# Kernel tuning notes

Hardware: AMD Instinct MI355X
Metric: run time of the kernel (lower is better)

## Reference

```python
import jax, jax.numpy as jnp
import numpy as np
from jax import lax

N = 2; C_IN = 256
H0, W0 = 100, 152
H1, W1 = 50, 76
DYN_CH = 34            # 4 init_offset + 4 bound_pt_offset + 18 semantic_pt_offset + 8 reg_aggr_attn
REG_CH = 4             # 4 boundary points x 1 channel each
NUM_CLASSES = 80
SEM_PTS = 9
CLS_CH = SEM_PTS * NUM_CLASSES
BOUND_PTS = 4
RATIO = 0.5            # LIMIT_BOUND_POINT_OFFSET_RATIO

_BASE = np.array([[1,0,0,0],[0,1,0,0],[0.5,0,0.5,0],
                  [0,0.5,0,0.5],[0,0,1,0],[0,0,0,1]], np.float32)
BOUND_MAT = jnp.asarray(_BASE[[0,3,2,1,4,3,2,5]])                      # (8,4) box -> cross-shaped 4 pts
SEM_MAT = jnp.asarray(_BASE[[0,1,0,3,0,5,2,1,2,3,2,5,4,1,4,3,4,5]])    # (18,4) box -> 3x3 pts
BOUND_OFF_IDX = jnp.array([1, 2, 5, 6])   # tangential coordinate channel of each boundary point
LOC_IDX = jnp.array([0, 3, 4, 7])         # box-side coordinate channel of each boundary point

def conv3x3(x, w, b):
    y = lax.conv_general_dilated(x, w, (1, 1), 'SAME',
                                 dimension_numbers=('NCHW', 'OIHW', 'NCHW'))
    return y + b[None, :, None, None]

def conv1x1(x, w):
    return jnp.einsum('oi,nihw->nohw', w[:, :, 0, 0], x)

def pred_collect(fmap, pts, point_num, reduce_points, bias=None):
    # Bilinearly sample per-point channel groups of fmap at dynamic point locations.
    # fmap: (N, P*c, Hm, Wm); pts: (N, 2P, H, W) with (x, y) pairs per point.
    Nb, C, Hm, Wm = fmap.shape
    P = point_num; c = C // P
    H, W = pts.shape[2], pts.shape[3]
    fm = fmap.reshape(Nb, P, c, Hm, Wm)
    pg = pts.reshape(Nb, P, 2, H, W)
    def sample(f, pt):  # f: (c, Hm, Wm), pt: (2, H, W)
        x = jnp.clip(pt[0], 0.0, Wm - 1.0)
        y = jnp.clip(pt[1], 0.0, Hm - 1.0)
        x0 = jnp.floor(x); y0 = jnp.floor(y)
        fx = x - x0; fy = y - y0
        x0i = x0.astype(jnp.int32); y0i = y0.astype(jnp.int32)
        x1i = jnp.minimum(x0i + 1, Wm - 1); y1i = jnp.minimum(y0i + 1, Hm - 1)
        v00 = f[:, y0i, x0i]; v01 = f[:, y0i, x1i]
        v10 = f[:, y1i, x0i]; v11 = f[:, y1i, x1i]
        return v00*(1-fx)*(1-fy) + v01*fx*(1-fy) + v10*(1-fx)*fy + v11*fx*fy
    vals = jax.vmap(jax.vmap(sample))(fm, pg)  # (N, P, c, H, W)
    if reduce_points:
        out = vals.sum(axis=1)
        if bias is not None:
            out = out + bias[None, :, None, None]
        return out
    return vals.reshape(Nb, P * c, H, W)

def head_forward(reg_feats, cls_feats, anchors, dyn_w, dyn_b, reg_w, cls_w, cls_b):
    reg_maps = [conv1x1(x, reg_w) for x in reg_feats]
    cls_maps = [conv1x1(x, cls_w) for x in cls_feats]
    cls_scores, coarse_boxes, reg_boxes = [], [], []
    for i, (reg_feat, anchor) in enumerate(zip(reg_feats, anchors)):
        Nb, _, H, W = reg_feat.shape
        pred = conv3x3(reg_feat, dyn_w, dyn_b)
        init_off, bpt_off, spt_off, attn = jnp.split(pred, [4, 8, 26], axis=1)
        coarse = anchor + init_off                                  # (N,4,H,W) = (x1,y1,x2,y2)
        # straight-through clamp of boundary-point tangential offsets to +-wh/2*ratio
        bpt_off = bpt_off.reshape(Nb, 2, 2, 1, H, W)
        wh = jnp.stack([coarse[:, 3] - coarse[:, 1],
                        coarse[:, 2] - coarse[:, 0]], axis=1) / 2 * RATIO  # (N,2,H,W) [h,w]
        thres = wh[:, None, :, None]                                # (N,1,2,1,H,W)
        extra = jnp.maximum(bpt_off - thres, 0.0) + jnp.minimum(bpt_off + thres, 0.0)
        bpt_off = (bpt_off - lax.stop_gradient(extra)).reshape(Nb, 4, H, W)
        bound_pt = lax.stop_gradient(jnp.einsum('oc,nchw->nohw', BOUND_MAT, coarse))
        bound_pt = bound_pt.at[:, BOUND_OFF_IDX].add(bpt_off)       # (N,8,H,W)
        bound_pt_loc = bound_pt[:, LOC_IDX]                         # (N,4,H,W)
        reg_val = pred_collect(reg_maps[i], bound_pt, BOUND_PTS, False)  # (N,4,H,W)
        if i > 0:
            attn_sm = jax.nn.softmax(attn.reshape(Nb, BOUND_PTS, 2, H, W), axis=2)
            reg_hi = reg_val.reshape(Nb, BOUND_PTS, 1, 1, H, W)
            reg_lo = pred_collect(reg_maps[i - 1], bound_pt * 2, BOUND_PTS, False)
            reg_lo = reg_lo.reshape(Nb, BOUND_PTS, 1, 1, H, W) * 0.5
            reg_val = (jnp.concatenate([reg_lo, reg_hi], axis=2)
                       * attn_sm[:, :, :, None]).sum(axis=2).reshape(Nb, -1, H, W)
        reg_box = (lax.stop_gradient(bound_pt_loc) + reg_val).reshape(Nb, 4, -1, H, W).mean(axis=2)
        sem_pt = lax.stop_gradient(jnp.einsum('oc,nchw->nohw', SEM_MAT, coarse)) + spt_off
        cls_score = pred_collect(cls_maps[i], sem_pt, SEM_PTS, True, cls_b)  # (N,80,H,W)
        cls_scores.append(cls_score); coarse_boxes.append(coarse); reg_boxes.append(reg_box)
    return cls_scores, coarse_boxes, reg_boxes

def make_anchor(H, W):
    gy, gx = jnp.meshgrid(jnp.arange(H, dtype=jnp.float32),
                          jnp.arange(W, dtype=jnp.float32), indexing='ij')
    a = jnp.stack([gx - 4.0, gy - 4.0, gx + 4.0, gy + 4.0], axis=0)
    return jnp.broadcast_to(a[None], (N, 4, H, W))

def setup_inputs() -> dict:
    key = jax.random.key(0)
    ks = jax.random.split(key, 7)
    return {
        "reg_feat0": jax.random.normal(ks[0], (N, C_IN, H0, W0), jnp.float32),
        "reg_feat1": jax.random.normal(ks[1], (N, C_IN, H1, W1), jnp.float32),
        "cls_feat0": jax.random.normal(ks[2], (N, C_IN, H0, W0), jnp.float32),
        "cls_feat1": jax.random.normal(ks[3], (N, C_IN, H1, W1), jnp.float32),
        "anchor0": make_anchor(H0, W0),
        "anchor1": make_anchor(H1, W1),
        "dyn_w": jax.random.normal(ks[4], (DYN_CH, C_IN, 3, 3), jnp.float32) * 0.01,
        "dyn_b": jnp.zeros((DYN_CH,), jnp.float32),
        "reg_w": jax.random.normal(ks[5], (REG_CH, C_IN, 1, 1), jnp.float32) * 0.05,
        "cls_w": jax.random.normal(ks[6], (CLS_CH, C_IN, 1, 1), jnp.float32) * 0.05,
        "cls_b": jnp.zeros((NUM_CLASSES,), jnp.float32),
    }

def reference(reg_feat0, reg_feat1, cls_feat0, cls_feat1, anchor0, anchor1,
              dyn_w, dyn_b, reg_w, cls_w, cls_b):
    cls_scores, coarse_boxes, reg_boxes = head_forward(
        [reg_feat0, reg_feat1], [cls_feat0, cls_feat1], [anchor0, anchor1],
        dyn_w, dyn_b, reg_w, cls_w, cls_b)
    return (*cls_scores, *coarse_boxes, *reg_boxes)
```

## Files before the change

kernel.cpp:

```cpp
#include <hip/hip_runtime.h>
#include <hip/hip_bf16.h>
#include <cstdint>

#define N_BATCH 2
#define C_IN 256
#define DYN_CH 34
#define CLS_CH 720
#define NUM_CLASSES 80
#define NCOMB 48

#define P0c 15200
#define P1c 3800
#define M0c 30400
#define M1c 7600
#define MT0c 119
#define MT1c 30
#define CT0c 475
#define CT1c 119

typedef __attribute__((ext_vector_type(8))) short short8;
typedef __attribute__((ext_vector_type(4))) float f32x4;

typedef const unsigned int __attribute__((address_space(1)))* gas1_t;
typedef unsigned int __attribute__((address_space(3)))* las3_t;

__device__ __forceinline__ void async_ld16(const void* g, void* l) {
  __builtin_amdgcn_global_load_lds((gas1_t)g, (las3_t)l, 16, 0, 0);
}

__global__ __launch_bounds__(256) void pack_feat(
    const float* __restrict__ cls0, const float* __restrict__ cls1,
    const float* __restrict__ reg0, const float* __restrict__ reg1,
    const float* __restrict__ cls_w, const float* __restrict__ dyn_w,
    const float* __restrict__ reg_w, __hip_bfloat16* __restrict__ a0,
    __hip_bfloat16* __restrict__ a1, __hip_bfloat16* __restrict__ r0,
    __hip_bfloat16* __restrict__ r1, __hip_bfloat16* __restrict__ bpack,
    __hip_bfloat16* __restrict__ wpack) {
  int b = blockIdx.x;
  if (b >= 2384) {
    b -= 2384;
    if (b < 90) {
      int u = b * 256 + threadIdx.x;
      if (u >= 9 * 32 * 80) return;
      int ntile = u / 2560;
      int rem = u % 2560;
      int kcg = rem / 80;
      int ochl = rem % 80;
      int och = ntile * 80 + ochl;
      const float* wr = cls_w + (size_t)och * C_IN + kcg * 8;
      __hip_bfloat16 tmp[8];
#pragma unroll
      for (int c = 0; c < 8; ++c) tmp[c] = __float2bfloat16(wr[c]);
      *(uint4*)(bpack + (size_t)u * 8) = *(const uint4*)tmp;
    } else {
      int u = (b - 90) * 256 + threadIdx.x;
      if (u >= 13824) return;
      int j = u / 768;
      int r = u % 768;
      int n = r / 16;
      int s = r % 16;
      int ku = j * 16 + (s ^ (n & 7));
      int k0 = ku * 8;
      int tap = k0 >> 8;
      int c0 = k0 & 255;
      __hip_bfloat16 tmp[8];
#pragma unroll
      for (int i = 0; i < 8; ++i) {
        int c = c0 + i;
        float v = 0.f;
        if (n < DYN_CH) v = dyn_w[((size_t)n * C_IN + c) * 9 + tap];
        else if (n < DYN_CH + 4 && tap == 4)
          v = reg_w[(size_t)(n - DYN_CH) * C_IN + c];
        tmp[i] = __float2bfloat16(v);
      }
      *(uint4*)(wpack + (size_t)u * 8) = *(const uint4*)tmp;
    }
    return;
  }
  int j = b & 7;
  int mtg = b >> 3;
  const float* src;
  __hip_bfloat16* dst;
  int P, Mtot, mtile;
  if (mtg < 119)      { src = cls0; dst = a0; P = P0c; Mtot = M0c; mtile = mtg; }
  else if (mtg < 149) { src = cls1; dst = a1; P = P1c; Mtot = M1c; mtile = mtg - 119; }
  else if (mtg < 268) { src = reg0; dst = r0; P = P0c; Mtot = M0c; mtile = mtg - 149; }
  else                { src = reg1; dst = r1; P = P1c; Mtot = M1c; mtile = mtg - 268; }
  int wave = threadIdx.x >> 6;
  int lane = threadIdx.x & 63;
  int kcg = j * 4 + wave;
  int c0 = kcg * 8;
  int m4 = mtile * 256 + lane * 4;
  uint4* du = (uint4*)dst + (size_t)mtile * 8192 + (size_t)kcg * 256 + lane * 4;
  if (m4 < Mtot) {
    int n = m4 / P;
    int p = m4 - n * P;
    const float* sp = src + ((size_t)n * C_IN + c0) * P + p;
    float4 f[8];
#pragma unroll
    for (int c = 0; c < 8; ++c) f[c] = *(const float4*)(sp + (size_t)c * P);
#pragma unroll
    for (int i = 0; i < 4; ++i) {
      union { uint4 u; __hip_bfloat16 h[8]; } o;
#pragma unroll
      for (int c = 0; c < 8; ++c) {
        float v = (i == 0) ? f[c].x : (i == 1) ? f[c].y : (i == 2) ? f[c].z : f[c].w;
        o.h[c] = __float2bfloat16(v);
      }
      du[i] = o.u;
    }
  } else {
    uint4 z = {0u, 0u, 0u, 0u};
#pragma unroll
    for (int i = 0; i < 4; ++i) du[i] = z;
  }
}

__global__ __launch_bounds__(256) void cls_gemm_mfma(
    const uint4* __restrict__ Ap0, const uint4* __restrict__ Ap1,
    const uint4* __restrict__ Bp, __hip_bfloat16* __restrict__ out0,
    __hip_bfloat16* __restrict__ out1) {
  __shared__ uint4 Ash[1024];
  __shared__ uint4 Bsh[320];
  int bb = blockIdx.x;
  int g = bb & 7;
  int loc = bb >> 3;
  int lm = loc / 9;
  int ntile = loc - lm * 9;
  int mtile = g * 19 + lm;
  if (mtile >= MT0c + MT1c) return;
  int tid = threadIdx.x;
  int wave = tid >> 6;
  int lane = tid & 63;
  int l15 = lane & 15;
  int kq = lane >> 4;

  const uint4* Ap;
  __hip_bfloat16* out;
  int Mtot;
  if (mtile < MT0c) { Ap = Ap0; out = out0; Mtot = M0c; }
  else              { mtile -= MT0c; Ap = Ap1; out = out1; Mtot = M1c; }

  const uint4* Ab = Ap + (size_t)mtile * 8192;
  const uint4* Bb = Bp + (size_t)ntile * 2560;

  f32x4 acc[4][5];
#pragma unroll
  for (int i = 0; i < 4; ++i)
#pragma unroll
    for (int j = 0; j < 5; ++j) acc[i][j] = (f32x4)0.f;

  for (int kb = 0; kb < 8; ++kb) {
    const uint4* Aslab = Ab + kb * 1024;
#pragma unroll
    for (int i = 0; i < 4; ++i) {
      int j = wave * 4 + i;
      async_ld16(Aslab + j * 64 + lane, &Ash[j * 64]);
    }
    const uint4* Bslab = Bb + kb * 320;
    for (int j = wave; j < 5; j += 4) {
      async_ld16(Bslab + j * 64 + lane, &Bsh[j * 64]);
    }
    __syncthreads();

    short8 a[4], b[5];
    const uint4* Ar = &Ash[kq * 256 + wave * 64 + l15];
#pragma unroll
    for (int mi = 0; mi < 4; ++mi) a[mi] = *(const short8*)&Ar[mi * 16];
    const uint4* Br = &Bsh[kq * 80 + l15];
#pragma unroll
    for (int ni = 0; ni < 5; ++ni) b[ni] = *(const short8*)&Br[ni * 16];
#pragma unroll
    for (int mi = 0; mi < 4; ++mi)
#pragma unroll
      for (int ni = 0; ni < 5; ++ni)
        acc[mi][ni] = __builtin_amdgcn_mfma_f32_16x16x32_bf16(
            a[mi], b[ni], acc[mi][ni], 0, 0, 0);
    __syncthreads();
  }

  int gbase = mtile * 256 + wave * 64;
#pragma unroll
  for (int mi = 0; mi < 4; ++mi) {
#pragma unroll
    for (int r = 0; r < 4; ++r) {
      int gg = gbase + mi * 16 + kq * 4 + r;
      if (gg >= Mtot) continue;
      __hip_bfloat16* orow = out + (size_t)gg * CLS_CH + ntile * 80 + l15;
#pragma unroll
      for (int ni = 0; ni < 5; ++ni)
        orow[ni * 16] = __float2bfloat16(acc[mi][ni][r]);
    }
  }
}

__global__ __launch_bounds__(256) void dyn_reg_conv_mfma(
    const uint4* __restrict__ rp0, const uint4* __restrict__ rp1,
    const uint4* __restrict__ wp, float* __restrict__ part0,
    float* __restrict__ part1) {
  __shared__ uint4 Bs[768];
  int tid = threadIdx.x;
  int wave = tid >> 6;
  int lane = tid & 63;
  int l15 = lane & 15;
  int kq = lane >> 4;
  int seg = blockIdx.y;
  int bx = blockIdx.x;

  const uint4* rp;
  float* part;
  int Mtot, P, W, H;
  if (bx < CT0c) { rp = rp0; part = part0; Mtot = M0c; P = P0c; W = 152; H = 100; }
  else { bx -= CT0c; rp = rp1; part = part1; Mtot = M1c; P = P1c; W = 76; H = 50; }

  int m = bx * 64 + wave * 16 + l15;
  bool mval = (m < Mtot);
  int mc = mval ? m : 0;
  int n = mc / P;
  int rem = mc - n * P;
  int y = rem / W;
  int x = rem - y * W;

  f32x4 acc[3];
#pragma unroll
  for (int i = 0; i < 3; ++i) acc[i] = (f32x4)0.f;

  for (int jj = 0; jj < 6; ++jj) {
    int j = seg * 6 + jj;
    const uint4* wsrc = wp + (size_t)j * 768 + wave * 192;
#pragma unroll
    for (int i = 0; i < 3; ++i)
      async_ld16(wsrc + i * 64 + lane, &Bs[wave * 192 + i * 64]);

    int tap = j >> 1;
    int cb8 = (j & 1) * 16;
    int dy = tap / 3 - 1, dx = tap % 3 - 1;
    int sy = y + dy, sx = x + dx;
    bool val = mval && ((unsigned)sy < (unsigned)H) && ((unsigned)sx < (unsigned)W);
    int sm = m + dy * W + dx;
    int smc = val ? sm : 0;
    size_t tbase = (size_t)(smc >> 8) * 8192 + (smc & 255);
    uint4 a[4];
#pragma unroll
    for (int t = 0; t < 4; ++t) {
      uint4 v = {0u, 0u, 0u, 0u};
      if (val) v = rp[tbase + (size_t)(cb8 + t * 4 + kq) * 256];
      a[t] = v;
    }
    __syncthreads();
#pragma unroll
    for (int t = 0; t < 4; ++t) {
#pragma unroll
      for (int ni = 0; ni < 3; ++ni) {
        int nn = ni * 16 + l15;
        short8 bf = *(const short8*)&Bs[nn * 16 + ((t * 4 + kq) ^ (nn & 7))];
        acc[ni] = __builtin_amdgcn_mfma_f32_16x16x32_bf16(
            *(short8*)&a[t], bf, acc[ni], 0, 0, 0);
      }
    }
    __syncthreads();
  }

  int mrow = bx * 64 + wave * 16 + kq * 4;
#pragma unroll
  for (int r = 0; r < 4; ++r) {
    int mm = mrow + r;
    if (mm >= Mtot) continue;
    float* dst = part + ((size_t)seg * Mtot + mm) * NCOMB + l15;
#pragma unroll
    for (int ni = 0; ni < 3; ++ni) dst[ni * 16] = acc[ni][r];
  }
}

__device__ __forceinline__ float samp48(const float* __restrict__ part,
                                        int Mtot, int nbase, int W, int H,
                                        float px, float py, int ch) {
  float xc = fminf(fmaxf(px, 0.f), (float)(W - 1));
  float yc = fminf(fmaxf(py, 0.f), (float)(H - 1));
  float x0f = floorf(xc), y0f = floorf(yc);
  float fx = xc - x0f, fy = yc - y0f;
  int x0 = (int)x0f, y0 = (int)y0f;
  int x1 = min(x0 + 1, W - 1), y1 = min(y0 + 1, H - 1);
  size_t m00 = (size_t)(nbase + y0 * W + x0);
  size_t m01 = (size_t)(nbase + y0 * W + x1);
  size_t m10 = (size_t)(nbase + y1 * W + x0);
  size_t m11 = (size_t)(nbase + y1 * W + x1);
  float v00 = 0.f, v01 = 0.f, v10 = 0.f, v11 = 0.f;
#pragma unroll
  for (int s = 0; s < 3; ++s) {
    size_t off = (size_t)s * Mtot;
    v00 += part[(off + m00) * NCOMB + ch];
    v01 += part[(off + m01) * NCOMB + ch];
    v10 += part[(off + m10) * NCOMB + ch];
    v11 += part[(off + m11) * NCOMB + ch];
  }
  return v00 * (1.f - fx) * (1.f - fy) + v01 * fx * (1.f - fy) +
         v10 * (1.f - fx) * fy + v11 * fx * fy;
}

__global__ __launch_bounds__(256) void decode(
    const float* __restrict__ part0, const float* __restrict__ part1,
    const float* __restrict__ dyn_b, const float* __restrict__ anchor0,
    const float* __restrict__ anchor1, float* __restrict__ out_coarse0,
    float* __restrict__ out_coarse1, float* __restrict__ out_regbox0,
    float* __restrict__ out_regbox1, int4* __restrict__ sidx0,
    float4* __restrict__ swt0, int4* __restrict__ sidx1,
    float4* __restrict__ swt1) {
  int bx = blockIdx.x;
  int n = blockIdx.y;
  const float* part;
  const float* anchor;
  float* out_coarse;
  float* out_regbox;
  int4* sidx;
  float4* swt;
  int Mtot, H, W, P, level;
  if (bx < 60) {
    part = part0; anchor = anchor0; out_coarse = out_coarse0;
    out_regbox = out_regbox0; sidx = sidx0; swt = swt0;
    Mtot = M0c; H = 100; W = 152; P = P0c; level = 0;
  } else {
    bx -= 60;
    part = part1; anchor = anchor1; out_coarse = out_coarse1;
    out_regbox = out_regbox1; sidx = sidx1; swt = swt1;
    Mtot = M1c; H = 50; W = 76; P = P1c; level = 1;
  }
  int p = bx * 256 + threadIdx.x;
  if (p >= P) return;
  int m = n * P + p;
  float pr[38];
  {
    const float* q0 = part + (size_t)m * NCOMB;
    const float* q1 = part + ((size_t)Mtot + m) * NCOMB;
    const float* q2 = part + ((size_t)2 * Mtot + m) * NCOMB;
#pragma unroll
    for (int o = 0; o < 38; ++o) pr[o] = q0[o] + q1[o] + q2[o];
#pragma unroll
    for (int o = 0; o < DYN_CH; ++o) pr[o] += dyn_b[o];
  }
  const float* an = anchor + (size_t)n * 4 * P + p;
  float cb[4];
#pragma unroll
  for (int k = 0; k < 4; ++k) cb[k] = an[(size_t)k * P] + pr[k];
  float* oc = out_coarse + (size_t)n * 4 * P + p;
#pragma unroll
  for (int k = 0; k < 4; ++k) oc[(size_t)k * P] = cb[k];

  float thr_y = (cb[3] - cb[1]) * 0.25f;
  float thr_x = (cb[2] - cb[0]) * 0.25f;
  float bo[4];
#pragma unroll
  for (int j = 0; j < 4; ++j) {
    float thr = (j & 1) ? thr_x : thr_y;
    float b = pr[4 + j];
    float extra = fmaxf(b - thr, 0.f) + fminf(b + thr, 0.f);
    bo[j] = b - extra;
  }
  float cx = 0.5f * (cb[0] + cb[2]);
  float cy = 0.5f * (cb[1] + cb[3]);
  float bp[8] = {cb[0], cy + bo[0], cx + bo[1], cb[1],
                 cb[2], cy + bo[2], cx + bo[3], cb[3]};

  int nbase = n * P;
  int nbaseLo = n * P0c;
  float rb[4];
#pragma unroll
  for (int pt = 0; pt < 4; ++pt) {
    float hi = samp48(part, Mtot, nbase, W, H, bp[2 * pt], bp[2 * pt + 1],
                      DYN_CH + pt);
    float val;
    if (level == 0) {
      val = hi;
    } else {
      float lo = 0.5f * samp48(part0, M0c, nbaseLo, 152, 100, bp[2 * pt] * 2.f,
                               bp[2 * pt + 1] * 2.f, DYN_CH + pt);
      float e0 = pr[26 + 2 * pt], e1 = pr[26 + 2 * pt + 1];
      float mx = fmaxf(e0, e1);
      float w0 = expf(e0 - mx), w1 = expf(e1 - mx);
      val = (lo * w0 + hi * w1) / (w0 + w1);
    }
    rb[pt] = val;
  }
  float* orb = out_regbox + (size_t)n * 4 * P + p;
  orb[0] = bp[0] + rb[0];
  orb[(size_t)P] = bp[3] + rb[1];
  orb[(size_t)2 * P] = bp[4] + rb[2];
  orb[(size_t)3 * P] = bp[7] + rb[3];

  float sx[9] = {cb[0], cb[0], cb[0], cx, cx, cx, cb[2], cb[2], cb[2]};
  float sy[9] = {cb[1], cy, cb[3], cb[1], cy, cb[3], cb[1], cy, cb[3]};
#pragma unroll
  for (int k = 0; k < 9; ++k) {
    float px = sx[k] + pr[8 + 2 * k];
    float py = sy[k] + pr[8 + 2 * k + 1];
    float xc = fminf(fmaxf(px, 0.f), (float)(W - 1));
    float yc = fminf(fmaxf(py, 0.f), (float)(H - 1));
    float x0f = floorf(xc), y0f = floorf(yc);
    float fx = xc - x0f, fy = yc - y0f;
    int x0 = (int)x0f, y0 = (int)y0f;
    int x1 = min(x0 + 1, W - 1), y1 = min(y0 + 1, H - 1);
    int4 iv;
    iv.x = (nbase + y0 * W + x0) * CLS_CH + k * 80;
    iv.y = (x1 - x0) * CLS_CH;
    iv.z = (y1 - y0) * W * CLS_CH;
    iv.w = 0;
    sidx[(size_t)k * Mtot + m] = iv;
    float4 wv = {(1.f - fx) * (1.f - fy), fx * (1.f - fy), (1.f - fx) * fy,
                 fx * fy};
    swt[(size_t)k * Mtot + m] = wv;
  }
}

__global__ __launch_bounds__(256) void cls_gather_f(
    const __hip_bfloat16* __restrict__ map0,
    const __hip_bfloat16* __restrict__ map1, const int4* __restrict__ sidx0,
    const float4* __restrict__ swt0, const int4* __restrict__ sidx1,
    const float4* __restrict__ swt1, const float* __restrict__ bias,
    float* __restrict__ outc0, float* __restrict__ outc1) {
  __shared__ float lds[NUM_CLASSES * 5];
  int b = (blockIdx.x & 7) * 1188 + (blockIdx.x >> 3);
  if (b >= 9500) return;
  const __hip_bfloat16* map;
  const int4* sidx;
  const float4* swt;
  float* out;
  int Mtot, P;
  if (b < 7600) { map = map0; sidx = sidx0; swt = swt0; out = outc0; Mtot = M0c; P = P0c; }
  else { b -= 7600; map = map1; sidx = sidx1; swt = swt1; out = outc1; Mtot = M1c; P = P1c; }
  int lane = threadIdx.x & 63;
  int wv = threadIdx.x >> 6;
  int m = b * 4 + wv;

  if (lane < 40) {
    int c2 = lane * 2;
    float ax = 0.f, ay = 0.f;
#pragma unroll
    for (int pt = 0; pt < 9; ++pt) {
      int4 iv = sidx[(size_t)pt * Mtot + m];
      float4 wt = swt[(size_t)pt * Mtot + m];
      const __hip_bfloat16* pl = map + iv.x + c2;
      unsigned t00 = *(const unsigned*)(pl);
      unsigned t01 = *(const unsigned*)(pl + iv.y);
      unsigned t10 = *(const unsigned*)(pl + iv.z);
      unsigned t11 = *(const unsigned*)(pl + iv.y + iv.z);
      ax += wt.x * __uint_as_float(t00 << 16) +
            wt.y * __uint_as_float(t01 << 16) +
            wt.z * __uint_as_float(t10 << 16) +
            wt.w * __uint_as_float(t11 << 16);
      ay += wt.x * __uint_as_float(t00 & 0xffff0000u) +
            wt.y * __uint_as_float(t01 & 0xffff0000u) +
            wt.z * __uint_as_float(t10 & 0xffff0000u) +
            wt.w * __uint_as_float(t11 & 0xffff0000u);
    }
    lds[c2 * 5 + wv] = ax;
    lds[(c2 + 1) * 5 + wv] = ay;
  }
  __syncthreads();
  int tid = threadIdx.x;
  if (tid < NUM_CLASSES) {
    float bb = bias[tid];
    float4 v = {lds[tid * 5] + bb, lds[tid * 5 + 1] + bb, lds[tid * 5 + 2] + bb,
                lds[tid * 5 + 3] + bb};
    int m0 = b * 4;
    int n = m0 / P;
    int p0 = m0 - n * P;
    *(float4*)&out[((size_t)n * NUM_CLASSES + tid) * P + p0] = v;
  }
}

extern "C" void kernel_launch(void* const* d_in, const int* in_sizes, int n_in,
                              void* d_out, int out_size, void* d_ws,
                              size_t ws_size, hipStream_t stream) {
  const float* reg_feat0 = (const float*)d_in[0];
  const float* reg_feat1 = (const float*)d_in[1];
  const float* cls_feat0 = (const float*)d_in[2];
  const float* cls_feat1 = (const float*)d_in[3];
  const float* anchor0 = (const float*)d_in[4];
  const float* anchor1 = (const float*)d_in[5];
  const float* dyn_w = (const float*)d_in[6];
  const float* dyn_b = (const float*)d_in[7];
  const float* reg_w = (const float*)d_in[8];
  const float* cls_w = (const float*)d_in[9];
  const float* cls_b = (const float*)d_in[10];

  float* out = (float*)d_out;
  float* out_cls0 = out;
  float* out_cls1 = out_cls0 + (size_t)N_BATCH * NUM_CLASSES * P0c;
  float* out_coarse0 = out_cls1 + (size_t)N_BATCH * NUM_CLASSES * P1c;
  float* out_coarse1 = out_coarse0 + (size_t)N_BATCH * 4 * P0c;
  float* out_reg0 = out_coarse1 + (size_t)N_BATCH * 4 * P1c;
  float* out_reg1 = out_reg0 + (size_t)N_BATCH * 4 * P0c;

  char* w = (char*)d_ws;
  __hip_bfloat16* bpack = (__hip_bfloat16*)w;   w += 368640;
  __hip_bfloat16* wpack = (__hip_bfloat16*)w;   w += 221184;
  char* apack_base = w;
  __hip_bfloat16* apack0 = (__hip_bfloat16*)w;  w += 15597568;
  __hip_bfloat16* apack1 = (__hip_bfloat16*)w;  w += 3932160;
  char* rpack_base = w;
  __hip_bfloat16* rpack0 = (__hip_bfloat16*)w;  w += 15597568;
  __hip_bfloat16* rpack1 = (__hip_bfloat16*)w;  w += 3932160;
  float* part1 = (float*)w;                     w += 4377600;
  __hip_bfloat16* map0 = (__hip_bfloat16*)w;    w += 43776000;
  __hip_bfloat16* map1 = (__hip_bfloat16*)w;    w += 10944000;
  float* part0 = (float*)apack_base;
  int4* sidx0 = (int4*)rpack_base;
  float4* swt0 = (float4*)(rpack_base + 4377600);
  int4* sidx1 = (int4*)(rpack_base + 8755200);
  float4* swt1 = (float4*)(rpack_base + 9849600);

  hipLaunchKernelGGL(pack_feat, dim3(2528), dim3(256), 0, stream, cls_feat0,
                     cls_feat1, reg_feat0, reg_feat1, cls_w, dyn_w, reg_w,
                     apack0, apack1, rpack0, rpack1, bpack, wpack);
  hipLaunchKernelGGL(cls_gemm_mfma, dim3(8 * 19 * 9), dim3(256), 0, stream,
                     (const uint4*)apack0, (const uint4*)apack1,
                     (const uint4*)bpack, map0, map1);
  hipLaunchKernelGGL(dyn_reg_conv_mfma, dim3(CT0c + CT1c, 3), dim3(256), 0,
                     stream, (const uint4*)rpack0, (const uint4*)rpack1,
                     (const uint4*)wpack, part0, part1);
  hipLaunchKernelGGL(decode, dim3(75, N_BATCH), dim3(256), 0, stream, part0,
                     part1, dyn_b, anchor0, anchor1, out_coarse0, out_coarse1,
                     out_reg0, out_reg1, sidx0, swt0, sidx1, swt1);
  hipLaunchKernelGGL(cls_gather_f, dim3(9504), dim3(256), 0, stream, map0,
                     map1, sidx0, swt0, sidx1, swt1, cls_b, out_cls0, out_cls1);
}
```

Measured before the change: 246.3 us.

## Spread gather lanes across points and vectorize decode loads with smaller blocks

Result: faster. 237.6 us (-3.5%).

```diff
diff --git a/kernel.cpp b/kernel.cpp
--- a/kernel.cpp
+++ b/kernel.cpp
@@ -298,7 +298,7 @@
          v10 * (1.f - fx) * fy + v11 * fx * fy;
 }
 
-__global__ __launch_bounds__(256) void decode(
+__global__ __launch_bounds__(64) void decode(
     const float* __restrict__ part0, const float* __restrict__ part1,
     const float* __restrict__ dyn_b, const float* __restrict__ anchor0,
     const float* __restrict__ anchor1, float* __restrict__ out_coarse0,
@@ -315,26 +315,32 @@
   int4* sidx;
   float4* swt;
   int Mtot, H, W, P, level;
-  if (bx < 60) {
+  if (bx < 238) {
     part = part0; anchor = anchor0; out_coarse = out_coarse0;
     out_regbox = out_regbox0; sidx = sidx0; swt = swt0;
     Mtot = M0c; H = 100; W = 152; P = P0c; level = 0;
   } else {
-    bx -= 60;
+    bx -= 238;
     part = part1; anchor = anchor1; out_coarse = out_coarse1;
     out_regbox = out_regbox1; sidx = sidx1; swt = swt1;
     Mtot = M1c; H = 50; W = 76; P = P1c; level = 1;
   }
-  int p = bx * 256 + threadIdx.x;
+  int p = bx * 64 + threadIdx.x;
   if (p >= P) return;
   int m = n * P + p;
-  float pr[38];
+  float pr[40];
   {
-    const float* q0 = part + (size_t)m * NCOMB;
-    const float* q1 = part + ((size_t)Mtot + m) * NCOMB;
-    const float* q2 = part + ((size_t)2 * Mtot + m) * NCOMB;
-#pragma unroll
-    for (int o = 0; o < 38; ++o) pr[o] = q0[o] + q1[o] + q2[o];
+    const float4* q0 = (const float4*)(part + (size_t)m * NCOMB);
+    const float4* q1 = (const float4*)(part + ((size_t)Mtot + m) * NCOMB);
+    const float4* q2 = (const float4*)(part + ((size_t)2 * Mtot + m) * NCOMB);
+#pragma unroll
+    for (int o4 = 0; o4 < 10; ++o4) {
+      float4 a = q0[o4], b = q1[o4], c = q2[o4];
+      pr[4 * o4 + 0] = a.x + b.x + c.x;
+      pr[4 * o4 + 1] = a.y + b.y + c.y;
+      pr[4 * o4 + 2] = a.z + b.z + c.z;
+      pr[4 * o4 + 3] = a.w + b.w + c.w;
+    }
 #pragma unroll
     for (int o = 0; o < DYN_CH; ++o) pr[o] += dyn_b[o];
   }
@@ -431,29 +437,55 @@
   int wv = threadIdx.x >> 6;
   int m = b * 4 + wv;
 
-  if (lane < 40) {
-    int c2 = lane * 2;
-    float ax = 0.f, ay = 0.f;
-#pragma unroll
-    for (int pt = 0; pt < 9; ++pt) {
-      int4 iv = sidx[(size_t)pt * Mtot + m];
-      float4 wt = swt[(size_t)pt * Mtot + m];
-      const __hip_bfloat16* pl = map + iv.x + c2;
-      unsigned t00 = *(const unsigned*)(pl);
-      unsigned t01 = *(const unsigned*)(pl + iv.y);
-      unsigned t10 = *(const unsigned*)(pl + iv.z);
-      unsigned t11 = *(const unsigned*)(pl + iv.y + iv.z);
-      ax += wt.x * __uint_as_float(t00 << 16) +
-            wt.y * __uint_as_float(t01 << 16) +
-            wt.z * __uint_as_float(t10 << 16) +
-            wt.w * __uint_as_float(t11 << 16);
-      ay += wt.x * __uint_as_float(t00 & 0xffff0000u) +
-            wt.y * __uint_as_float(t01 & 0xffff0000u) +
-            wt.z * __uint_as_float(t10 & 0xffff0000u) +
-            wt.w * __uint_as_float(t11 & 0xffff0000u);
-    }
-    lds[c2 * 5 + wv] = ax;
-    lds[(c2 + 1) * 5 + wv] = ay;
+  int sub = lane / 20;
+  if (sub > 2) sub = 2;
+  int cl = lane - (lane / 20 > 2 ? 40 : (lane / 20) * 20);
+  cl = lane % 20;
+  int c4 = cl * 4;
+
+  float a0 = 0.f, a1 = 0.f, a2 = 0.f, a3 = 0.f;
+#pragma unroll
+  for (int g = 0; g < 3; ++g) {
+    int pt = g * 3 + sub;
+    int4 iv = sidx[(size_t)pt * Mtot + m];
+    float4 wt = swt[(size_t)pt * Mtot + m];
+    const __hip_bfloat16* pl = map + iv.x + c4;
+    uint2 t00 = *(const uint2*)(pl);
+    uint2 t01 = *(const uint2*)(pl + iv.y);
+    uint2 t10 = *(const uint2*)(pl + iv.z);
+    uint2 t11 = *(const uint2*)(pl + iv.y + iv.z);
+    a0 += wt.x * __uint_as_float(t00.x << 16) +
+          wt.y * __uint_as_float(t01.x << 16) +
+          wt.z * __uint_as_float(t10.x << 16) +
+          wt.w * __uint_as_float(t11.x << 16);
+    a1 += wt.x * __uint_as_float(t00.x & 0xffff0000u) +
+          wt.y * __uint_as_float(t01.x & 0xffff0000u) +
+          wt.z * __uint_as_float(t10.x & 0xffff0000u) +
+          wt.w * __uint_as_float(t11.x & 0xffff0000u);
+    a2 += wt.x * __uint_as_float(t00.y << 16) +
+          wt.y * __uint_as_float(t01.y << 16) +
+          wt.z * __uint_as_float(t10.y << 16) +
+          wt.w * __uint_as_float(t11.y << 16);
+    a3 += wt.x * __uint_as_float(t00.y & 0xffff0000u) +
+          wt.y * __uint_as_float(t01.y & 0xffff0000u) +
+          wt.z * __uint_as_float(t10.y & 0xffff0000u) +
+          wt.w * __uint_as_float(t11.y & 0xffff0000u);
+  }
+  {
+    float s0 = __shfl(a0, lane + 20), u0 = __shfl(a0, lane + 40);
+    float s1 = __shfl(a1, lane + 20), u1 = __shfl(a1, lane + 40);
+    float s2 = __shfl(a2, lane + 20), u2 = __shfl(a2, lane + 40);
+    float s3 = __shfl(a3, lane + 20), u3 = __shfl(a3, lane + 40);
+    a0 += s0 + u0;
+    a1 += s1 + u1;
+    a2 += s2 + u2;
+    a3 += s3 + u3;
+  }
+  if (lane < 20) {
+    lds[(c4 + 0) * 5 + wv] = a0;
+    lds[(c4 + 1) * 5 + wv] = a1;
+    lds[(c4 + 2) * 5 + wv] = a2;
+    lds[(c4 + 3) * 5 + wv] = a3;
   }
   __syncthreads();
   int tid = threadIdx.x;
@@ -518,7 +550,7 @@
   hipLaunchKernelGGL(dyn_reg_conv_mfma, dim3(CT0c + CT1c, 3), dim3(256), 0,
                      stream, (const uint4*)rpack0, (const uint4*)rpack1,
                      (const uint4*)wpack, part0, part1);
-  hipLaunchKernelGGL(decode, dim3(75, N_BATCH), dim3(256), 0, stream, part0,
+  hipLaunchKernelGGL(decode, dim3(298, N_BATCH), dim3(64), 0, stream, part0,
                      part1, dyn_b, anchor0, anchor1, out_coarse0, out_coarse1,
                      out_reg0, out_reg1, sidx0, swt0, sidx1, swt1);
   hipLaunchKernelGGL(cls_gather_f, dim3(9504), dim3(256), 0, stream, map0,
```
